# Kernel tuning notes

Measured on AMD Instinct MI355X. Metric: run time of the kernel, lower is better.

The kernel has to match this reference:

```python
import jax, jax.numpy as jnp
import numpy as np

N, E, B = 16384, 131072, 256
F_IN, HID, HEADS, F_CELL, N_OUT = 78, 128, 10, 954, 2
NEG_SLOPE = 0.2  # PyG GATConv default


def setup_inputs() -> dict:
    key = jax.random.key(0)
    ks = jax.random.split(key, 24)
    rn = lambda k, shape, s=0.05: (jax.random.normal(k, shape, jnp.float32) * s)
    inp = {
        "x": rn(ks[0], (N, F_IN), 1.0),
        "edge_index": jax.random.randint(ks[1], (2, E), 0, N, dtype=jnp.int32),
        "batch": (jnp.arange(N, dtype=jnp.int32) // (N // B)),  # 64 nodes per graph, sorted
        "cell": rn(ks[2], (B, F_CELL), 1.0),
        "W1": rn(ks[3], (F_IN, HEADS * HID)),
        "a_src1": rn(ks[4], (HEADS, HID)),
        "a_dst1": rn(ks[5], (HEADS, HID)),
        "b1": jnp.zeros((HEADS * HID,), jnp.float32),
        # GATConv layer 2: 1280 -> 128, 1 head
        "W2": rn(ks[6], (HEADS * HID, HID)),
        "a_src2": rn(ks[7], (1, HID)),
        "a_dst2": rn(ks[8], (1, HID)),
        "b2": jnp.zeros((HID,), jnp.float32),
        # drug1_fc_g1: 128 -> 128
        "Wg": rn(ks[9], (HID, HID)), "bg": jnp.zeros((HID,), jnp.float32),
        # fc head applied to normalized cell (source applies fc1 to cell: 954 -> 2048)
        "Wf1": rn(ks[10], (F_CELL, 2048)), "bf1": jnp.zeros((2048,), jnp.float32),
        "Wf2": rn(ks[11], (2048, 512)), "bf2": jnp.zeros((512,), jnp.float32),
        "Wf3": rn(ks[12], (512, 128)), "bf3": jnp.zeros((128,), jnp.float32),
        "Wo": rn(ks[13], (128, N_OUT)), "bo": jnp.zeros((N_OUT,), jnp.float32),
    }
    return inp


def _gat_layer(xin, src, dst, W, a_s, a_d, b, heads, ch):
    """PyG GATConv: linear -> per-edge leaky_relu(a_src.h_j + a_dst.h_i) ->
    segment softmax over incoming edges of dst -> scatter-add of alpha * h_src."""
    n = xin.shape[0]
    h = (xin @ W).reshape(n, heads, ch)                       # [N,H,C]
    es = jnp.einsum('nhc,hc->nh', h, a_s)                     # alpha_src per node
    ed = jnp.einsum('nhc,hc->nh', h, a_d)                     # alpha_dst per node
    e = jax.nn.leaky_relu(es[src] + ed[dst], NEG_SLOPE)       # [Etot,H]
    m = jax.ops.segment_max(e, dst, num_segments=n)           # stable softmax max
    w = jnp.exp(e - m[dst])                                   # unnormalized alpha
    denom = jax.ops.segment_sum(w, dst, num_segments=n)       # [N,H]
    num = jax.ops.segment_sum(w[:, :, None] * h[src], dst, num_segments=n)  # [N,H,C]
    out = num / denom[:, :, None]
    return out.reshape(n, heads * ch) + b


def reference(x, edge_index, batch, cell, W1, a_src1, a_dst1, b1,
              W2, a_src2, a_dst2, b2, Wg, bg, Wf1, bf1, Wf2, bf2,
              Wf3, bf3, Wo, bo):
    n = x.shape[0]
    # add self-loops (PyG GATConv default)
    loop = jnp.arange(n, dtype=edge_index.dtype)
    src = jnp.concatenate([edge_index[0], loop])
    dst = jnp.concatenate([edge_index[1], loop])

    x1 = jax.nn.elu(_gat_layer(x, src, dst, W1, a_src1, a_dst1, b1, HEADS, HID))
    x1 = jax.nn.elu(_gat_layer(x1, src, dst, W2, a_src2, a_dst2, b2, 1, HID))
    # global max pool over graphs (batch is sorted, all B segments non-empty)
    x1 = jax.ops.segment_max(x1, batch, num_segments=B)       # [B,128]
    x1 = jax.nn.relu(x1 @ Wg + bg)

    # cell branch: L2 normalize rows, then dense head (dropout = identity in eval)
    celln = cell / jnp.maximum(jnp.linalg.norm(cell, axis=1, keepdims=True), 1e-12)
    xc = jax.nn.relu(celln @ Wf1 + bf1)
    xc = jax.nn.relu(xc @ Wf2 + bf2)
    xc = jax.nn.relu(xc @ Wf3 + bf3)
    out = xc @ Wo + bo                                        # [B,2]
    # source returns only `out`; we also expose the (otherwise-dead) GAT branch
    return jnp.concatenate([x1, out], axis=1)                 # [B,130]
```

## Files before the change

### kernel.cpp

```cpp
#include <hip/hip_runtime.h>
#include <hip/hip_bf16.h>
#include <math.h>

#define N_NODES 16384
#define E_EDGES 131072
#define ETOT (E_EDGES + N_NODES)
#define BGRAPH 256
#define F_INPUT 78
#define KPAD1 96
#define HID 128
#define HEADS 10
#define F1 (HEADS * HID)
#define F_CELL 954
#define KPADC 960
#define NEG_SLOPE 0.2f

typedef __attribute__((ext_vector_type(8))) short frag_t;
typedef __attribute__((ext_vector_type(4))) float f4_t;

static __device__ __forceinline__ unsigned fkey(float f) {
    unsigned b = __float_as_uint(f);
    return (b & 0x80000000u) ? ~b : (b | 0x80000000u);
}
static __device__ __forceinline__ float funkey(unsigned k) {
    unsigned b = (k & 0x80000000u) ? (k ^ 0x80000000u) : ~k;
    return __uint_as_float(b);
}
static __device__ __forceinline__ unsigned short f2bf(float f) {
    __hip_bfloat16 h = __float2bfloat16(f);
    return *(unsigned short*)&h;
}
static __device__ __forceinline__ float bf2f(unsigned short u) {
    return __uint_as_float(((unsigned)u) << 16);
}

template<int WM16, int WN16, int OUT_MODE, int ACT, int HAS_BIAS>
__global__ __launch_bounds__(256) void mfma_gemm(
    const unsigned short* __restrict__ A, const unsigned short* __restrict__ BT,
    const float* __restrict__ bias, void* __restrict__ C,
    float* __restrict__ esp, float* __restrict__ edp,
    const float* __restrict__ ca, const float* __restrict__ cd,
    int M, int N, int Kpad, int lda, int ldc,
    int za, int zb, int zc, int zbias)
{
    constexpr int BM = 32 * WM16, BN = 32 * WN16;
    __shared__ __align__(16) unsigned short Als[BM * 32];
    __shared__ __align__(16) unsigned short Bls[BN * 32];
    const int z = blockIdx.z;
    A  += (size_t)z * za;
    BT += (size_t)z * zb;
    const int t = threadIdx.x;
    const int wave = t >> 6, lane = t & 63;
    const int wr = (wave >> 1) * (16 * WM16);
    const int wc = (wave & 1) * (16 * WN16);
    const int row0 = blockIdx.y * BM;
    const int col0 = blockIdx.x * BN;

    f4_t acc[WM16][WN16];
#pragma unroll
    for (int m = 0; m < WM16; m++)
#pragma unroll
        for (int n = 0; n < WN16; n++) { acc[m][n] = (f4_t){0.f, 0.f, 0.f, 0.f}; }

    const int lrow = lane & 15, kg = lane >> 4;
    for (int kk = 0; kk < Kpad; kk += 32) {
        for (int i = t; i < BM * 4; i += 256) {
            int r = i >> 2, slot = i & 3;
            uint4 v = *(const uint4*)&A[(size_t)(row0 + r) * lda + kk + slot * 8];
            *(uint4*)&Als[r * 32 + ((slot ^ (r & 3) ^ ((r >> 2) & 3)) * 8)] = v;
        }
        for (int i = t; i < BN * 4; i += 256) {
            int r = i >> 2, slot = i & 3;
            uint4 v = *(const uint4*)&BT[(size_t)(col0 + r) * Kpad + kk + slot * 8];
            *(uint4*)&Bls[r * 32 + ((slot ^ (r & 3) ^ ((r >> 2) & 3)) * 8)] = v;
        }
        __syncthreads();
        frag_t af[WM16], bfr[WN16];
#pragma unroll
        for (int m = 0; m < WM16; m++) {
            int r = wr + m * 16 + lrow;
            af[m] = *(frag_t*)&Als[r * 32 + ((kg ^ (r & 3) ^ ((r >> 2) & 3)) * 8)];
        }
#pragma unroll
        for (int n = 0; n < WN16; n++) {
            int r = wc + n * 16 + lrow;
            bfr[n] = *(frag_t*)&Bls[r * 32 + ((kg ^ (r & 3) ^ ((r >> 2) & 3)) * 8)];
        }
#pragma unroll
        for (int m = 0; m < WM16; m++)
#pragma unroll
            for (int n = 0; n < WN16; n++)
                acc[m][n] = __builtin_amdgcn_mfma_f32_16x16x32_bf16(af[m], bfr[n], acc[m][n], 0, 0, 0);
        __syncthreads();
    }

    if constexpr (OUT_MODE <= 2) {
#pragma unroll
        for (int m = 0; m < WM16; m++) {
#pragma unroll
            for (int n = 0; n < WN16; n++) {
                int col = col0 + wc + n * 16 + lrow;
                float bv = HAS_BIAS ? bias[z * zbias + col] : 0.f;
#pragma unroll
                for (int r = 0; r < 4; r++) {
                    int row = row0 + wr + m * 16 + kg * 4 + r;
                    float v = acc[m][n][r] + bv;
                    if (ACT == 1) v = fmaxf(v, 0.f);
                    if (ACT == 2) v = (v > 0.f) ? v : expm1f(v);
                    size_t ci = (size_t)row * ldc + (size_t)z * zc + col;
                    if (OUT_MODE == 0)      ((float*)C)[ci] = v;
                    else if (OUT_MODE == 1) ((unsigned short*)C)[ci] = f2bf(v);
                    else {
                        if (col < 10)                  esp[row * 10 + col] = v;
                        else if (col >= 16 && col < 26) edp[row * 10 + (col - 16)] = v;
                    }
                }
            }
        }
    } else if constexpr (OUT_MODE == 3) {
        __shared__ float esl[BM], edl[BM];
        if (t < BM) { esl[t] = 0.f; edl[t] = 0.f; }
        __syncthreads();
#pragma unroll
        for (int r = 0; r < 4; r++) {
            int lr = wr + kg * 4 + r;
            float pes = 0.f, ped = 0.f;
#pragma unroll
            for (int n = 0; n < WN16; n++) {
                int col = col0 + wc + n * 16 + lrow;
                float v = acc[0][n][r];
                ((unsigned short*)C)[(size_t)(row0 + lr) * ldc + col] = f2bf(v);
                pes = fmaf(v, ca[col], pes);
                ped = fmaf(v, cd[col], ped);
            }
            atomicAdd(&esl[lr], pes);
            atomicAdd(&edl[lr], ped);
        }
        __syncthreads();
        if (t < BM) { esp[row0 + t] = esl[t]; edp[row0 + t] = edl[t]; }
    } else {
        __shared__ float o2l[BM][2];
        if (t < BM) { o2l[t][0] = 0.f; o2l[t][1] = 0.f; }
        __syncthreads();
#pragma unroll
        for (int m = 0; m < WM16; m++) {
#pragma unroll
            for (int r = 0; r < 4; r++) {
                int lr = wr + m * 16 + kg * 4 + r;
                float p0 = 0.f, p1 = 0.f;
#pragma unroll
                for (int n = 0; n < WN16; n++) {
                    int col = col0 + wc + n * 16 + lrow;
                    float v = acc[m][n][r] + (HAS_BIAS ? bias[col] : 0.f);
                    if (ACT == 1) v = fmaxf(v, 0.f);
                    p0 = fmaf(v, ca[col * 2], p0);
                    p1 = fmaf(v, ca[col * 2 + 1], p1);
                }
                atomicAdd(&o2l[lr][0], p0);
                atomicAdd(&o2l[lr][1], p1);
            }
        }
        __syncthreads();
        if (t < BM) {
            ((float*)C)[(size_t)(row0 + t) * ldc + 128] = o2l[t][0] + cd[0];
            ((float*)C)[(size_t)(row0 + t) * ldc + 129] = o2l[t][1] + cd[1];
        }
    }
}

#define S0 1572864
#define S1 122880
#define S2 163840
#define S3 1966080
#define S4 1048576
#define S5 65536
#define S6 16384
#define PREP_TOTAL (S0+S1+S2+S3+S4+S5+S6)
#define NB_ELEM (PREP_TOTAL / 256)
#define NB_FOLD 768
#define NB_ZCNT 64
#define NB_ZPK  128

__global__ void prep_all(const float* __restrict__ x,  const float* __restrict__ W1,
                         const float* __restrict__ W2, const float* __restrict__ Wf1,
                         const float* __restrict__ Wf2, const float* __restrict__ Wf3,
                         const float* __restrict__ Wg,
                         const float* __restrict__ as1, const float* __restrict__ ad1,
                         unsigned short* __restrict__ xb,  unsigned short* __restrict__ W1T,
                         unsigned short* __restrict__ W2T, unsigned short* __restrict__ Wf1T,
                         unsigned short* __restrict__ Wf2T, unsigned short* __restrict__ Wf3T,
                         unsigned short* __restrict__ WgT, unsigned short* __restrict__ F1T,
                         int* __restrict__ counts, unsigned* __restrict__ pk)
{
    int blk = blockIdx.x, t = threadIdx.x;
    if (blk < NB_ELEM) {
        int i = blk * 256 + t;
        if (i < S0) { int r = i / 96, k = i % 96;
            xb[i] = (k < F_INPUT) ? f2bf(x[r * F_INPUT + k]) : 0; return; }
        i -= S0;
        if (i < S1) { int n = i / 96, k = i % 96;
            W1T[i] = (k < F_INPUT) ? f2bf(W1[(size_t)k * F1 + n]) : 0; return; }
        i -= S1;
        if (i < S2) { int n = i / 1280, k = i % 1280;
            W2T[i] = f2bf(W2[(size_t)k * HID + n]); return; }
        i -= S2;
        if (i < S3) { int n = i / 960, k = i % 960;
            Wf1T[i] = (k < F_CELL) ? f2bf(Wf1[(size_t)k * 2048 + n]) : 0; return; }
        i -= S3;
        if (i < S4) { int n = i / 2048, k = i % 2048;
            Wf2T[i] = f2bf(Wf2[(size_t)k * 512 + n]); return; }
        i -= S4;
        if (i < S5) { int n = i / 512, k = i % 512;
            Wf3T[i] = f2bf(Wf3[(size_t)k * HID + n]); return; }
        i -= S5;
        { int n = i / 128, k = i % 128;
            WgT[i] = f2bf(Wg[(size_t)k * HID + n]); }
        return;
    }
    blk -= NB_ELEM;
    if (blk < NB_FOLD) {
        int idx = blk * 4 + (t >> 6);
        int l = t & 63;
        int r = idx / 96, k = idx % 96;
        int sd = r >> 4, h = r & 15;
        float p = 0.f;
        if (h < HEADS && k < F_INPUT) {
            const float* a = (sd ? ad1 : as1) + h * HID;
            float2 wv = *(const float2*)&W1[(size_t)k * F1 + h * HID + 2 * l];
            float2 av = *(const float2*)&a[2 * l];
            p = wv.x * av.x + wv.y * av.y;
#pragma unroll
            for (int o = 32; o > 0; o >>= 1) p += __shfl_xor(p, o);
        }
        if (l == 0) F1T[(size_t)r * 96 + k] = f2bf(p);
        return;
    }
    blk -= NB_FOLD;
    if (blk < NB_ZCNT) { counts[blk * 256 + t] = 0; return; }
    blk -= NB_ZCNT;
    pk[blk * 256 + t] = 0;
}

__global__ void hist_dst(const int* __restrict__ ei, int* __restrict__ counts)
{
    int e = blockIdx.x * blockDim.x + threadIdx.x;
    if (e >= ETOT) return;
    int dst = (e < E_EDGES) ? ei[E_EDGES + e] : (e - E_EDGES);
    atomicAdd(&counts[dst], 1);
}

__global__ void scan_counts(const int* __restrict__ counts,
                            int* __restrict__ row_start, int* __restrict__ cursor)
{
    __shared__ int part[256];
    int t = threadIdx.x;
    int base = t * 64;
    int sum = 0;
    for (int i = 0; i < 64; i++) sum += counts[base + i];
    part[t] = sum;
    __syncthreads();
    for (int o = 1; o < 256; o <<= 1) {
        int v = 0;
        if (t >= o) v = part[t - o];
        __syncthreads();
        part[t] += v;
        __syncthreads();
    }
    int run = (t == 0) ? 0 : part[t - 1];
    for (int i = 0; i < 64; i++) {
        row_start[base + i] = run;
        cursor[base + i] = run;
        run += counts[base + i];
    }
    if (t == 255) row_start[N_NODES] = run;
}

__global__ void scatter_csr(const int* __restrict__ ei, int* __restrict__ cursor,
                            int* __restrict__ csr_src)
{
    int e = blockIdx.x * blockDim.x + threadIdx.x;
    if (e >= ETOT) return;
    int src, dst;
    if (e < E_EDGES) { src = ei[e]; dst = ei[E_EDGES + e]; } else { src = dst = e - E_EDGES; }
    int pos = atomicAdd(&cursor[dst], 1);
    csr_src[pos] = src;
}

__global__ __launch_bounds__(256) void gat1_agg(
    const int* __restrict__ row_start, const int* __restrict__ csr_src,
    const unsigned* __restrict__ xb32,
    const float* __restrict__ es, const float* __restrict__ ed,
    unsigned* __restrict__ aggb)
{
    const int w = threadIdx.x >> 6, l = threadIdx.x & 63;
    const int n = blockIdx.x * 4 + w;
    const int rs = row_start[n];
    const int deg = row_start[n + 1] - rs;

    __shared__ __align__(16) float w_lds[4][64][12];
    __shared__ int src_lds[4][64];

    float edv[HEADS];
    const float* edp = ed + n * HEADS;
#pragma unroll
    for (int h = 0; h < HEADS; h++) edv[h] = edp[h];

    float acc0[HEADS], acc1[HEADS], den[HEADS];
#pragma unroll
    for (int h = 0; h < HEADS; h++) { acc0[h] = 0.f; acc1[h] = 0.f; den[h] = 0.f; }

    for (int base = 0; base < deg; base += 64) {
        int e = base + l;
        int cnt = min(64, deg - base);
        float wv[HEADS];
        if (e < deg) {
            int s = csr_src[rs + e];
            src_lds[w][l] = s;
            const float* ep = es + s * HEADS;
#pragma unroll
            for (int h = 0; h < HEADS; h++) {
                float v = ep[h] + edv[h];
                v = (v >= 0.f) ? v : NEG_SLOPE * v;
                wv[h] = __expf(v);
            }
        } else {
#pragma unroll
            for (int h = 0; h < HEADS; h++) wv[h] = 0.f;
        }
#pragma unroll
        for (int h = 0; h < HEADS; h++) {
            den[h] += wv[h];
            w_lds[w][l][h] = wv[h];
        }
        asm volatile("" ::: "memory");

        for (int j = 0; j < cnt; j++) {
            int sj = src_lds[w][j];
            unsigned xv = 0;
            if (l < 48) xv = xb32[(size_t)sj * 48 + l];
            float x0 = bf2f((unsigned short)(xv & 0xffffu));
            float x1v = bf2f((unsigned short)(xv >> 16));
            float4 wa = *(const float4*)&w_lds[w][j][0];
            float4 wb = *(const float4*)&w_lds[w][j][4];
            float2 wcv = *(const float2*)&w_lds[w][j][8];
            float ww[HEADS] = {wa.x, wa.y, wa.z, wa.w, wb.x, wb.y, wb.z, wb.w, wcv.x, wcv.y};
#pragma unroll
            for (int h = 0; h < HEADS; h++) {
                acc0[h] = fmaf(ww[h], x0, acc0[h]);
                acc1[h] = fmaf(ww[h], x1v, acc1[h]);
            }
        }
        asm volatile("" ::: "memory");
    }

#pragma unroll
    for (int h = 0; h < HEADS; h++)
#pragma unroll
        for (int o = 32; o > 0; o >>= 1) den[h] += __shfl_xor(den[h], o);

    if (l < 48) {
        unsigned* orow = aggb + (size_t)n * 480;
#pragma unroll
        for (int h = 0; h < HEADS; h++) {
            float inv = 1.f / den[h];
            unsigned lo = f2bf(acc0[h] * inv);
            unsigned hi = f2bf(acc1[h] * inv);
            orow[h * 48 + l] = lo | (hi << 16);
        }
    }
}

__global__ __launch_bounds__(256) void gat2_agg(
    const int* __restrict__ row_start, const int* __restrict__ csr_src,
    const unsigned short* __restrict__ H2,
    const float* __restrict__ es, const float* __restrict__ ed,
    const float* __restrict__ b, const int* __restrict__ batch,
    unsigned* __restrict__ pk)
{
    const int w = threadIdx.x >> 6, l = threadIdx.x & 63;
    const int n = blockIdx.x * 4 + w;
    const int rs = row_start[n];
    const int deg = row_start[n + 1] - rs;
    const float edv = ed[n];

    float2 acc = {0.f, 0.f};
    float den = 0.f;
    for (int base = 0; base < deg; base += 64) {
        int e = base + l;
        int cnt = min(64, deg - base);
        int s = 0;
        float wv = 0.f;
        if (e < deg) {
            s = csr_src[rs + e];
            float v = es[s] + edv;
            v = (v >= 0.f) ? v : NEG_SLOPE * v;
            wv = __expf(v);
        }
        den += wv;
        for (int j = 0; j < cnt; j++) {
            float wj = __shfl(wv, j);
            int   sj = __shfl(s, j);
            unsigned hp = *(const unsigned*)&H2[(size_t)sj * HID + 2 * l];
            acc.x = fmaf(wj, bf2f((unsigned short)(hp & 0xffffu)), acc.x);
            acc.y = fmaf(wj, bf2f((unsigned short)(hp >> 16)), acc.y);
        }
    }
#pragma unroll
    for (int o = 32; o > 0; o >>= 1) den += __shfl_xor(den, o);

    float inv = 1.f / den;
    float2 bv = *(const float2*)&b[2 * l];
    float v0 = acc.x * inv + bv.x;
    float v1 = acc.y * inv + bv.y;
    v0 = (v0 > 0.f) ? v0 : expm1f(v0);
    v1 = (v1 > 0.f) ? v1 : expm1f(v1);
    int g = batch[n];
    atomicMax(&pk[g * HID + 2 * l], fkey(v0));
    atomicMax(&pk[g * HID + 2 * l + 1], fkey(v1));
}

__global__ void decode_cell(const unsigned* __restrict__ pk,
                            unsigned short* __restrict__ pooledb,
                            const float* __restrict__ cell,
                            unsigned short* __restrict__ celln)
{
    int t = threadIdx.x;
    if (blockIdx.x < BGRAPH) {
        int b = blockIdx.x;
        __shared__ float red[256];
        float s = 0.f;
        for (int c = t; c < F_CELL; c += 256) { float v = cell[(size_t)b * F_CELL + c]; s += v * v; }
        red[t] = s; __syncthreads();
        for (int o = 128; o > 0; o >>= 1) { if (t < o) red[t] += red[t + o]; __syncthreads(); }
        float inv = 1.f / fmaxf(sqrtf(red[0]), 1e-12f);
        for (int c = t; c < KPADC; c += 256) {
            float v = (c < F_CELL) ? cell[(size_t)b * F_CELL + c] * inv : 0.f;
            celln[(size_t)b * KPADC + c] = f2bf(v);
        }
    } else {
        int i = (blockIdx.x - BGRAPH) * 256 + t;
        if (i < BGRAPH * HID) pooledb[i] = f2bf(funkey(pk[i]));
    }
}

extern "C" void kernel_launch(void* const* d_in, const int* in_sizes, int n_in,
                              void* d_out, int out_size, void* d_ws, size_t ws_size,
                              hipStream_t stream)
{
    const float* x    = (const float*)d_in[0];
    const int*   ei   = (const int*)d_in[1];
    const int*   batch= (const int*)d_in[2];
    const float* cell = (const float*)d_in[3];
    const float* W1   = (const float*)d_in[4];
    const float* as1  = (const float*)d_in[5];
    const float* ad1  = (const float*)d_in[6];
    const float* b1   = (const float*)d_in[7];
    const float* W2   = (const float*)d_in[8];
    const float* as2  = (const float*)d_in[9];
    const float* ad2  = (const float*)d_in[10];
    const float* b2   = (const float*)d_in[11];
    const float* Wg   = (const float*)d_in[12];
    const float* bg   = (const float*)d_in[13];
    const float* Wf1  = (const float*)d_in[14];
    const float* bf1  = (const float*)d_in[15];
    const float* Wf2  = (const float*)d_in[16];
    const float* bf2  = (const float*)d_in[17];
    const float* Wf3  = (const float*)d_in[18];
    const float* bf3  = (const float*)d_in[19];
    const float* Wo   = (const float*)d_in[20];
    const float* bo   = (const float*)d_in[21];
    float* out = (float*)d_out;

    char* w = (char*)d_ws;
    auto alloc = [&](size_t bytes) { char* p = w; w += (bytes + 255) & ~(size_t)255; return p; };
    unsigned short* xb   = (unsigned short*)alloc((size_t)N_NODES * KPAD1 * 2);
    unsigned short* W1T  = (unsigned short*)alloc((size_t)F1 * KPAD1 * 2);
    unsigned short* F1T  = (unsigned short*)alloc((size_t)32 * KPAD1 * 2);
    unsigned*       aggb = (unsigned*)alloc((size_t)N_NODES * 480 * 4);
    unsigned short* x1   = (unsigned short*)alloc((size_t)N_NODES * F1 * 2);
    unsigned short* W2T  = (unsigned short*)alloc((size_t)HID * F1 * 2);
    unsigned short* H2   = (unsigned short*)alloc((size_t)N_NODES * HID * 2);
    float*    es1  = (float*)alloc((size_t)N_NODES * HEADS * 4);
    float*    ed1  = (float*)alloc((size_t)N_NODES * HEADS * 4);
    float*    es2  = (float*)alloc((size_t)N_NODES * 4);
    float*    ed2  = (float*)alloc((size_t)N_NODES * 4);
    int*      counts    = (int*)alloc((size_t)N_NODES * 4);
    int*      row_start = (int*)alloc((size_t)(N_NODES + 1) * 4);
    int*      cursor    = (int*)alloc((size_t)N_NODES * 4);
    int*      csr_src   = (int*)alloc((size_t)ETOT * 4);
    unsigned* pk   = (unsigned*)alloc((size_t)BGRAPH * HID * 4);
    unsigned short* pooledb = (unsigned short*)alloc((size_t)BGRAPH * HID * 2);
    unsigned short* WgT  = (unsigned short*)alloc((size_t)HID * HID * 2);
    unsigned short* celln = (unsigned short*)alloc((size_t)BGRAPH * KPADC * 2);
    unsigned short* Wf1T = (unsigned short*)alloc((size_t)2048 * KPADC * 2);
    unsigned short* Wf2T = (unsigned short*)alloc((size_t)512 * 2048 * 2);
    unsigned short* Wf3T = (unsigned short*)alloc((size_t)HID * 512 * 2);
    unsigned short* xc1b = (unsigned short*)alloc((size_t)BGRAPH * 2048 * 2);
    unsigned short* xc2b = (unsigned short*)alloc((size_t)BGRAPH * 512 * 2);

    dim3 b256(256);
    const int egrid = (ETOT + 255) / 256;

    prep_all<<<NB_ELEM + NB_FOLD + NB_ZCNT + NB_ZPK, b256, 0, stream>>>(
        x, W1, W2, Wf1, Wf2, Wf3, Wg, as1, ad1,
        xb, W1T, W2T, Wf1T, Wf2T, Wf3T, WgT, F1T, counts, pk);

    hist_dst<<<egrid, b256, 0, stream>>>(ei, counts);
    scan_counts<<<1, b256, 0, stream>>>(counts, row_start, cursor);
    scatter_csr<<<egrid, b256, 0, stream>>>(ei, cursor, csr_src);

    mfma_gemm<4, 1, 2, 0, 0><<<dim3(1, N_NODES / 128), b256, 0, stream>>>(
        xb, F1T, nullptr, nullptr, es1, ed1, nullptr, nullptr,
        N_NODES, 32, KPAD1, KPAD1, 32, 0, 0, 0, 0);

    gat1_agg<<<N_NODES / 4, b256, 0, stream>>>(row_start, csr_src, (const unsigned*)xb,
                                               es1, ed1, aggb);

    mfma_gemm<4, 4, 1, 2, 1><<<dim3(1, N_NODES / 128, HEADS), b256, 0, stream>>>(
        (const unsigned short*)aggb, W1T, b1, x1, nullptr, nullptr, nullptr, nullptr,
        N_NODES, HID, KPAD1, 960, F1, KPAD1, HID * KPAD1, HID, HID);

    mfma_gemm<1, 4, 3, 0, 0><<<dim3(1, N_NODES / 32), b256, 0, stream>>>(
        x1, W2T, nullptr, H2, es2, ed2, as2, ad2,
        N_NODES, HID, F1, F1, HID, 0, 0, 0, 0);

    gat2_agg<<<N_NODES / 4, b256, 0, stream>>>(row_start, csr_src, H2, es2, ed2, b2,
                                               batch, pk);

    decode_cell<<<BGRAPH + (BGRAPH * HID + 255) / 256, b256, 0, stream>>>(
        pk, pooledb, cell, celln);

    mfma_gemm<2, 2, 0, 1, 1><<<dim3(HID / 64, BGRAPH / 64), b256, 0, stream>>>(
        pooledb, WgT, bg, out, nullptr, nullptr, nullptr, nullptr,
        BGRAPH, HID, HID, HID, 130, 0, 0, 0, 0);

    mfma_gemm<2, 2, 1, 1, 1><<<dim3(2048 / 64, BGRAPH / 64), b256, 0, stream>>>(
        celln, Wf1T, bf1, xc1b, nullptr, nullptr, nullptr, nullptr,
        BGRAPH, 2048, KPADC, KPADC, 2048, 0, 0, 0, 0);
    mfma_gemm<1, 2, 1, 1, 1><<<dim3(512 / 64, BGRAPH / 32), b256, 0, stream>>>(
        xc1b, Wf2T, bf2, xc2b, nullptr, nullptr, nullptr, nullptr,
        BGRAPH, 512, 2048, 2048, 512, 0, 0, 0, 0);

    mfma_gemm<2, 4, 4, 1, 1><<<dim3(1, BGRAPH / 64), b256, 0, stream>>>(
        xc2b, Wf3T, bf3, out, nullptr, nullptr, Wo, bo,
        BGRAPH, HID, 512, 512, 130, 0, 0, 0, 0);
}
```

Measured before the change: 253.1 us.

## Split-K the layer-2 GAT GEMM with atomic fp32 accumulation and separate convert kernel

The layer-2 projection GEMM (16384x1280 -> 128) is split four ways along K with blockIdx.z. Partial sums go into a zeroed fp32 buffer through atomicAdd, using larger 64-row tiles. A new h2_convert kernel then computes the attention logits es2/ed2 and packs H2 to bf16. The aim is more parallelism and better tile reuse than the old 32-row, full-K launch. The cost is an extra fp32 buffer that must be zeroed and read back, atomic traffic, and one more kernel launch.

```diff
diff --git a/kernel.cpp b/kernel.cpp
--- a/kernel.cpp
+++ b/kernel.cpp
@@ -40,7 +40,7 @@
     const float* __restrict__ bias, void* __restrict__ C,
     float* __restrict__ esp, float* __restrict__ edp,
     const float* __restrict__ ca, const float* __restrict__ cd,
-    int M, int N, int Kpad, int lda, int ldc,
+    int M, int N, int Kpad, int lda, int ldb, int ldc,
     int za, int zb, int zc, int zbias)
 {
     constexpr int BM = 32 * WM16, BN = 32 * WN16;
@@ -71,7 +71,7 @@
         }
         for (int i = t; i < BN * 4; i += 256) {
             int r = i >> 2, slot = i & 3;
-            uint4 v = *(const uint4*)&BT[(size_t)(col0 + r) * Kpad + kk + slot * 8];
+            uint4 v = *(const uint4*)&BT[(size_t)(col0 + r) * ldb + kk + slot * 8];
             *(uint4*)&Bls[r * 32 + ((slot ^ (r & 3) ^ ((r >> 2) & 3)) * 8)] = v;
         }
         __syncthreads();
@@ -94,7 +94,7 @@
         __syncthreads();
     }
 
-    if constexpr (OUT_MODE <= 2) {
+    if constexpr (OUT_MODE <= 2 || OUT_MODE == 5) {
 #pragma unroll
         for (int m = 0; m < WM16; m++) {
 #pragma unroll
@@ -110,6 +110,7 @@
                     size_t ci = (size_t)row * ldc + (size_t)z * zc + col;
                     if (OUT_MODE == 0)      ((float*)C)[ci] = v;
                     else if (OUT_MODE == 1) ((unsigned short*)C)[ci] = f2bf(v);
+                    else if (OUT_MODE == 5) atomicAdd(&((float*)C)[(size_t)row * ldc + col], acc[m][n][r]);
                     else {
                         if (col < 10)                  esp[row * 10 + col] = v;
                         else if (col >= 16 && col < 26) edp[row * 10 + (col - 16)] = v;
@@ -117,27 +118,6 @@
                 }
             }
         }
-    } else if constexpr (OUT_MODE == 3) {
-        __shared__ float esl[BM], edl[BM];
-        if (t < BM) { esl[t] = 0.f; edl[t] = 0.f; }
-        __syncthreads();
-#pragma unroll
-        for (int r = 0; r < 4; r++) {
-            int lr = wr + kg * 4 + r;
-            float pes = 0.f, ped = 0.f;
-#pragma unroll
-            for (int n = 0; n < WN16; n++) {
-                int col = col0 + wc + n * 16 + lrow;
-                float v = acc[0][n][r];
-                ((unsigned short*)C)[(size_t)(row0 + lr) * ldc + col] = f2bf(v);
-                pes = fmaf(v, ca[col], pes);
-                ped = fmaf(v, cd[col], ped);
-            }
-            atomicAdd(&esl[lr], pes);
-            atomicAdd(&edl[lr], ped);
-        }
-        __syncthreads();
-        if (t < BM) { esp[row0 + t] = esl[t]; edp[row0 + t] = edl[t]; }
     } else {
         __shared__ float o2l[BM][2];
         if (t < BM) { o2l[t][0] = 0.f; o2l[t][1] = 0.f; }
@@ -180,6 +160,7 @@
 #define NB_FOLD 768
 #define NB_ZCNT 64
 #define NB_ZPK  128
+#define NB_ZH2F 8192
 
 __global__ void prep_all(const float* __restrict__ x,  const float* __restrict__ W1,
                          const float* __restrict__ W2, const float* __restrict__ Wf1,
@@ -190,7 +171,8 @@
                          unsigned short* __restrict__ W2T, unsigned short* __restrict__ Wf1T,
                          unsigned short* __restrict__ Wf2T, unsigned short* __restrict__ Wf3T,
                          unsigned short* __restrict__ WgT, unsigned short* __restrict__ F1T,
-                         int* __restrict__ counts, unsigned* __restrict__ pk)
+                         int* __restrict__ counts, unsigned* __restrict__ pk,
+                         float* __restrict__ H2f)
 {
     int blk = blockIdx.x, t = threadIdx.x;
     if (blk < NB_ELEM) {
@@ -238,7 +220,9 @@
     blk -= NB_FOLD;
     if (blk < NB_ZCNT) { counts[blk * 256 + t] = 0; return; }
     blk -= NB_ZCNT;
-    pk[blk * 256 + t] = 0;
+    if (blk < NB_ZPK) { pk[blk * 256 + t] = 0; return; }
+    blk -= NB_ZPK;
+    H2f[(size_t)blk * 256 + t] = 0.f;
 }
 
 __global__ void hist_dst(const int* __restrict__ ei, int* __restrict__ counts)
@@ -284,6 +268,25 @@
     if (e < E_EDGES) { src = ei[e]; dst = ei[E_EDGES + e]; } else { src = dst = e - E_EDGES; }
     int pos = atomicAdd(&cursor[dst], 1);
     csr_src[pos] = src;
+}
+
+__global__ __launch_bounds__(256) void h2_convert(
+    const float* __restrict__ H2f, const float* __restrict__ as_,
+    const float* __restrict__ ad_, unsigned short* __restrict__ H2,
+    float* __restrict__ es, float* __restrict__ ed)
+{
+    int n = blockIdx.x * 4 + (threadIdx.x >> 6);
+    int l = threadIdx.x & 63;
+    float2 v = *(const float2*)&H2f[(size_t)n * HID + 2 * l];
+    float2 av = *(const float2*)&as_[2 * l];
+    float2 dv = *(const float2*)&ad_[2 * l];
+    float vs = v.x * av.x + v.y * av.y;
+    float vd = v.x * dv.x + v.y * dv.y;
+#pragma unroll
+    for (int o = 32; o > 0; o >>= 1) { vs += __shfl_xor(vs, o); vd += __shfl_xor(vd, o); }
+    if (l == 0) { es[n] = vs; ed[n] = vd; }
+    unsigned pw = (unsigned)f2bf(v.x) | ((unsigned)f2bf(v.y) << 16);
+    *(unsigned*)&H2[(size_t)n * HID + 2 * l] = pw;
 }
 
 __global__ __launch_bounds__(256) void gat1_agg(
@@ -479,6 +482,7 @@
     unsigned*       aggb = (unsigned*)alloc((size_t)N_NODES * 480 * 4);
     unsigned short* x1   = (unsigned short*)alloc((size_t)N_NODES * F1 * 2);
     unsigned short* W2T  = (unsigned short*)alloc((size_t)HID * F1 * 2);
+    float*          H2f  = (float*)alloc((size_t)N_NODES * HID * 4);
     unsigned short* H2   = (unsigned short*)alloc((size_t)N_NODES * HID * 2);
     float*    es1  = (float*)alloc((size_t)N_NODES * HEADS * 4);
     float*    ed1  = (float*)alloc((size_t)N_NODES * HEADS * 4);
@@ -501,9 +505,9 @@
     dim3 b256(256);
     const int egrid = (ETOT + 255) / 256;
 
-    prep_all<<<NB_ELEM + NB_FOLD + NB_ZCNT + NB_ZPK, b256, 0, stream>>>(
+    prep_all<<<NB_ELEM + NB_FOLD + NB_ZCNT + NB_ZPK + NB_ZH2F, b256, 0, stream>>>(
         x, W1, W2, Wf1, Wf2, Wf3, Wg, as1, ad1,
-        xb, W1T, W2T, Wf1T, Wf2T, Wf3T, WgT, F1T, counts, pk);
+        xb, W1T, W2T, Wf1T, Wf2T, Wf3T, WgT, F1T, counts, pk, H2f);
 
     hist_dst<<<egrid, b256, 0, stream>>>(ei, counts);
     scan_counts<<<1, b256, 0, stream>>>(counts, row_start, cursor);
@@ -511,18 +515,20 @@
 
     mfma_gemm<4, 1, 2, 0, 0><<<dim3(1, N_NODES / 128), b256, 0, stream>>>(
         xb, F1T, nullptr, nullptr, es1, ed1, nullptr, nullptr,
-        N_NODES, 32, KPAD1, KPAD1, 32, 0, 0, 0, 0);
+        N_NODES, 32, KPAD1, KPAD1, KPAD1, 32, 0, 0, 0, 0);
 
     gat1_agg<<<N_NODES / 4, b256, 0, stream>>>(row_start, csr_src, (const unsigned*)xb,
                                                es1, ed1, aggb);
 
     mfma_gemm<4, 4, 1, 2, 1><<<dim3(1, N_NODES / 128, HEADS), b256, 0, stream>>>(
         (const unsigned short*)aggb, W1T, b1, x1, nullptr, nullptr, nullptr, nullptr,
-        N_NODES, HID, KPAD1, 960, F1, KPAD1, HID * KPAD1, HID, HID);
-
-    mfma_gemm<1, 4, 3, 0, 0><<<dim3(1, N_NODES / 32), b256, 0, stream>>>(
-        x1, W2T, nullptr, H2, es2, ed2, as2, ad2,
-        N_NODES, HID, F1, F1, HID, 0, 0, 0, 0);
+        N_NODES, HID, KPAD1, 960, KPAD1, F1, KPAD1, HID * KPAD1, HID, HID);
+
+    mfma_gemm<2, 4, 5, 0, 0><<<dim3(1, N_NODES / 64, 4), b256, 0, stream>>>(
+        x1, W2T, nullptr, H2f, nullptr, nullptr, nullptr, nullptr,
+        N_NODES, HID, F1 / 4, F1, F1, HID, F1 / 4, F1 / 4, 0, 0);
+
+    h2_convert<<<N_NODES / 4, b256, 0, stream>>>(H2f, as2, ad2, H2, es2, ed2);
 
     gat2_agg<<<N_NODES / 4, b256, 0, stream>>>(row_start, csr_src, H2, es2, ed2, b2,
                                                batch, pk);
@@ -532,16 +538,16 @@
 
     mfma_gemm<2, 2, 0, 1, 1><<<dim3(HID / 64, BGRAPH / 64), b256, 0, stream>>>(
         pooledb, WgT, bg, out, nullptr, nullptr, nullptr, nullptr,
-        BGRAPH, HID, HID, HID, 130, 0, 0, 0, 0);
+        BGRAPH, HID, HID, HID, HID, 130, 0, 0, 0, 0);
 
     mfma_gemm<2, 2, 1, 1, 1><<<dim3(2048 / 64, BGRAPH / 64), b256, 0, stream>>>(
         celln, Wf1T, bf1, xc1b, nullptr, nullptr, nullptr, nullptr,
-        BGRAPH, 2048, KPADC, KPADC, 2048, 0, 0, 0, 0);
+        BGRAPH, 2048, KPADC, KPADC, KPADC, 2048, 0, 0, 0, 0);
     mfma_gemm<1, 2, 1, 1, 1><<<dim3(512 / 64, BGRAPH / 32), b256, 0, stream>>>(
         xc1b, Wf2T, bf2, xc2b, nullptr, nullptr, nullptr, nullptr,
-        BGRAPH, 512, 2048, 2048, 512, 0, 0, 0, 0);
+        BGRAPH, 512, 2048, 2048, 2048, 512, 0, 0, 0, 0);
 
     mfma_gemm<2, 4, 4, 1, 1><<<dim3(1, BGRAPH / 64), b256, 0, stream>>>(
         xc2b, Wf3T, bf3, out, nullptr, nullptr, Wo, bo,
-        BGRAPH, HID, 512, 512, 130, 0, 0, 0, 0);
-}
+        BGRAPH, HID, 512, 512, 512, 130, 0, 0, 0, 0);
+}
```

Result: no change. 253.1 us (-0.0%).
